# Performance work log

Measured on AMD Instinct MI355X. Metric: run time of the kernel, lower is better.

## Reference

```python
import jax, jax.numpy as jnp
import numpy as np

B, S, HLEN, VLEN, HID = 32, 2048, 1024, 1024, 1024


def setup_inputs() -> dict:
    key = jax.random.key(0)
    ks = jax.random.split(key, 6)
    scale_W = 1.0 / np.sqrt(HLEN)
    scale_U = 1.0 / np.sqrt(VLEN)
    scale_w = 1.0 / np.sqrt(HID)
    return {
        "h": jax.random.normal(ks[0], (B, HLEN), dtype=jnp.float32),
        "V": jax.random.normal(ks[1], (B, S, VLEN), dtype=jnp.float32),
        "W_w": jax.random.normal(ks[2], (HID, HLEN), dtype=jnp.float32) * scale_W,
        "W_b": jax.random.normal(ks[3], (HID,), dtype=jnp.float32) * scale_W,
        "U_w": jax.random.normal(ks[4], (HID, VLEN), dtype=jnp.float32) * scale_U,
        "w_w": jax.random.normal(ks[5], (HID,), dtype=jnp.float32) * scale_w,
    }


def reference(h, V, W_w, W_b, U_w, w_w):
    # e = w^T tanh(W h + U V^T + b); beta = softmax(e); out = sum_s beta_s V_s
    h_proj = h @ W_w.T + W_b                      # [B, HID]
    V_proj = jnp.einsum('bsv,dv->bsd', V, U_w)    # [B, S, HID]
    e = jnp.einsum('bsd,d->bs', jnp.tanh(h_proj[:, None, :] + V_proj), w_w)  # [B, S]
    beta = jax.nn.softmax(e, axis=1)              # [B, S]
    return jnp.einsum('bs,bsv->bv', beta, V)      # [B, VLEN]
```

## Files before the change

kernel.cpp:

```cpp
#include <hip/hip_runtime.h>

constexpr int B_   = 32;
constexpr int S_   = 2048;
constexpr int HID_ = 1024;
constexpr int VL_  = 1024;

typedef __attribute__((ext_vector_type(4))) float  f32x4;
typedef __attribute__((ext_vector_type(4))) short  s16x4;
typedef __attribute__((ext_vector_type(8))) short  s16x8;

__device__ __forceinline__ short f2bf(float f) {
    union { float f; unsigned u; } v; v.f = f;
    unsigned r = v.u + 0x7fffu + ((v.u >> 16) & 1u);
    return (short)(r >> 16);
}

__device__ __forceinline__ float bf2f(short s) {
    union { unsigned u; float f; } v;
    v.u = ((unsigned)(unsigned short)s) << 16;
    return v.f;
}

__device__ __forceinline__ float fast_tanh(float x) {
    float e2 = __expf(2.0f * x);
    return 1.0f - 2.0f / (e2 + 1.0f);
}

__device__ __forceinline__ void async_cp16(const void* g, void* l) {
    __builtin_amdgcn_global_load_lds(
        (const __attribute__((address_space(1))) unsigned int*)g,
        (__attribute__((address_space(3))) unsigned int*)l,
        16, 0, 0);
}

__global__ __launch_bounds__(256) void hproj_kernel(const float* __restrict__ h,
                                                    const float* __restrict__ Ww,
                                                    const float* __restrict__ Wb,
                                                    float* __restrict__ hp) {
    int tid = threadIdx.x;
    int wave = tid >> 6, lane = tid & 63;
    int d = blockIdx.x * 4 + wave;
    const float* wr = Ww + (size_t)d * HID_;
    float4 wreg[4];
#pragma unroll
    for (int i = 0; i < 4; i++) wreg[i] = *(const float4*)(wr + i * 256 + lane * 4);
    float bias = Wb[d];
    for (int b = 0; b < B_; b++) {
        const float* hr = h + (size_t)b * HID_;
        float acc = 0.0f;
#pragma unroll
        for (int i = 0; i < 4; i++) {
            float4 x = *(const float4*)(hr + i * 256 + lane * 4);
            acc += wreg[i].x * x.x + wreg[i].y * x.y + wreg[i].z * x.z + wreg[i].w * x.w;
        }
#pragma unroll
        for (int o = 32; o; o >>= 1) acc += __shfl_xor(acc, o);
        if (lane == 0) hp[(size_t)b * HID_ + d] = acc + bias;
    }
}

__global__ __launch_bounds__(256) void cvt_kernel(const float* __restrict__ src,
                                                  short* __restrict__ dst, size_t n4) {
    size_t i = (size_t)blockIdx.x * blockDim.x + threadIdx.x;
    size_t stride = (size_t)gridDim.x * blockDim.x;
    for (; i < n4; i += stride) {
        float4 x = ((const float4*)src)[i];
        s16x4 y;
        y.x = f2bf(x.x); y.y = f2bf(x.y); y.z = f2bf(x.z); y.w = f2bf(x.w);
        ((s16x4*)dst)[i] = y;
    }
}

__global__ __launch_bounds__(256) void e_kernel_bf16(const short* __restrict__ Vm,
                                                     const short* __restrict__ Um,
                                                     const float* __restrict__ hp,
                                                     const float* __restrict__ ww,
                                                     float* __restrict__ e) {
    __shared__ short As[128][32];
    __shared__ short Bs[128][32];
    __shared__ float ebuf[2][128];

    int tid = threadIdx.x;
    int s0 = blockIdx.x * 128;
    int b  = blockIdx.y;
    int wave = tid >> 6, lane = tid & 63;
    int wm = wave >> 1, wn = wave & 1;
    int col = lane & 15, quad = lane >> 4;

    int r0 = 32 * wave + (lane >> 2);
    int kc = (lane & 3) * 8;
    const short* gAb = Vm + ((size_t)b * S_ + s0 + r0) * VL_ + kc;
    short* lA0 = &As[32 * wave][0];
    short* lA1 = &As[32 * wave + 16][0];
    short* lB0 = &Bs[32 * wave][0];
    short* lB1 = &Bs[32 * wave + 16][0];

    float ep[4][4];
#pragma unroll
    for (int i = 0; i < 4; i++)
#pragma unroll
        for (int j = 0; j < 4; j++) ep[i][j] = 0.0f;

    for (int dt = 0; dt < 8; dt++) {
        int d0 = dt * 128;
        const short* gA0 = gAb;
        const short* gA1 = gAb + 16 * (size_t)VL_;
        const short* gB0 = Um + ((size_t)d0 + r0) * VL_ + kc;
        const short* gB1 = gB0 + 16 * (size_t)VL_;

        f32x4 zero = {0.f, 0.f, 0.f, 0.f};
        f32x4 acc[4][4];
#pragma unroll
        for (int i = 0; i < 4; i++)
#pragma unroll
            for (int j = 0; j < 4; j++) acc[i][j] = zero;

        for (int k0 = 0; k0 < VL_; k0 += 32) {
            async_cp16(gA0, lA0);
            async_cp16(gA1, lA1);
            async_cp16(gB0, lB0);
            async_cp16(gB1, lB1);
            gA0 += 32; gA1 += 32; gB0 += 32; gB1 += 32;
            __syncthreads();

            s16x8 a8[4], b8[4];
#pragma unroll
            for (int tm = 0; tm < 4; tm++)
                a8[tm] = *(const s16x8*)&As[wm * 64 + tm * 16 + col][quad * 8];
#pragma unroll
            for (int tn = 0; tn < 4; tn++)
                b8[tn] = *(const s16x8*)&Bs[wn * 64 + tn * 16 + col][quad * 8];
#pragma unroll
            for (int tm = 0; tm < 4; tm++)
#pragma unroll
                for (int tn = 0; tn < 4; tn++)
                    acc[tm][tn] = __builtin_amdgcn_mfma_f32_16x16x32_bf16(
                        a8[tm], b8[tn], acc[tm][tn], 0, 0, 0);
            __syncthreads();
        }

        float wv[4], hv[4];
#pragma unroll
        for (int tn = 0; tn < 4; tn++) {
            int d = d0 + wn * 64 + tn * 16 + col;
            wv[tn] = ww[d];
            hv[tn] = hp[(size_t)b * HID_ + d];
        }
#pragma unroll
        for (int tm = 0; tm < 4; tm++)
#pragma unroll
            for (int reg = 0; reg < 4; reg++) {
#pragma unroll
                for (int tn = 0; tn < 4; tn++)
                    ep[tm][reg] += wv[tn] * fast_tanh(hv[tn] + acc[tm][tn][reg]);
            }
    }

#pragma unroll
    for (int tm = 0; tm < 4; tm++)
#pragma unroll
        for (int reg = 0; reg < 4; reg++) {
            float p = ep[tm][reg];
            p += __shfl_xor(p, 1);
            p += __shfl_xor(p, 2);
            p += __shfl_xor(p, 4);
            p += __shfl_xor(p, 8);
            if (col == 0)
                ebuf[wn][wm * 64 + tm * 16 + quad * 4 + reg] = p;
        }
    __syncthreads();
    if (tid < 128)
        e[(size_t)b * S_ + s0 + tid] = ebuf[0][tid] + ebuf[1][tid];
}

__global__ __launch_bounds__(256) void e_kernel_f32(const float* __restrict__ Vm,
                                                    const float* __restrict__ Um,
                                                    const float* __restrict__ hp,
                                                    const float* __restrict__ ww,
                                                    float* __restrict__ e) {
    __shared__ short As[128][40];
    __shared__ short Bs[128][40];
    int tid = threadIdx.x;
    int b  = blockIdx.z;
    int d0 = blockIdx.x * 128;
    int s0 = blockIdx.y * 128;
    int wave = tid >> 6, lane = tid & 63;
    int wm = wave >> 1, wn = wave & 1;
    int col = lane & 15, quad = lane >> 4;

    f32x4 zero = {0.f, 0.f, 0.f, 0.f};
    f32x4 acc[4][4];
#pragma unroll
    for (int i = 0; i < 4; i++)
#pragma unroll
        for (int j = 0; j < 4; j++) acc[i][j] = zero;

    const float* Abase = Vm + ((size_t)b * S_ + s0) * (size_t)VL_;
    const float* Bbase = Um + (size_t)d0 * (size_t)VL_;

    for (int k0 = 0; k0 < VL_; k0 += 32) {
        int k4 = tid & 7, rb = tid >> 3;
#pragma unroll
        for (int i = 0; i < 4; i++) {
            int r = rb + 32 * i;
            float4 x = *(const float4*)(Abase + (size_t)r * VL_ + k0 + k4 * 4);
            s16x4 ya; ya.x = f2bf(x.x); ya.y = f2bf(x.y); ya.z = f2bf(x.z); ya.w = f2bf(x.w);
            *(s16x4*)&As[r][k4 * 4] = ya;
            float4 y = *(const float4*)(Bbase + (size_t)r * VL_ + k0 + k4 * 4);
            s16x4 yb; yb.x = f2bf(y.x); yb.y = f2bf(y.y); yb.z = f2bf(y.z); yb.w = f2bf(y.w);
            *(s16x4*)&Bs[r][k4 * 4] = yb;
        }
        __syncthreads();
        s16x8 a8[4], b8[4];
#pragma unroll
        for (int tm = 0; tm < 4; tm++)
            a8[tm] = *(const s16x8*)&As[wm * 64 + tm * 16 + col][quad * 8];
#pragma unroll
        for (int tn = 0; tn < 4; tn++)
            b8[tn] = *(const s16x8*)&Bs[wn * 64 + tn * 16 + col][quad * 8];
#pragma unroll
        for (int tm = 0; tm < 4; tm++)
#pragma unroll
            for (int tn = 0; tn < 4; tn++)
                acc[tm][tn] = __builtin_amdgcn_mfma_f32_16x16x32_bf16(
                    a8[tm], b8[tn], acc[tm][tn], 0, 0, 0);
        __syncthreads();
    }

    float wv[4], hv[4];
#pragma unroll
    for (int tn = 0; tn < 4; tn++) {
        int d = d0 + wn * 64 + tn * 16 + col;
        wv[tn] = ww[d];
        hv[tn] = hp[(size_t)b * HID_ + d];
    }
#pragma unroll
    for (int tm = 0; tm < 4; tm++) {
#pragma unroll
        for (int reg = 0; reg < 4; reg++) {
            float p = 0.0f;
#pragma unroll
            for (int tn = 0; tn < 4; tn++)
                p += wv[tn] * fast_tanh(hv[tn] + acc[tm][tn][reg]);
            p += __shfl_xor(p, 1);
            p += __shfl_xor(p, 2);
            p += __shfl_xor(p, 4);
            p += __shfl_xor(p, 8);
            if (col == 0) {
                int s = s0 + wm * 64 + tm * 16 + quad * 4 + reg;
                atomicAdd(&e[(size_t)b * S_ + s], p);
            }
        }
    }
}

__global__ __launch_bounds__(256) void softmax_kernel(float* __restrict__ e) {
    int b = blockIdx.x, tid = threadIdx.x;
    float* row = e + (size_t)b * S_;
    float v[8];
    float m = -1e30f;
#pragma unroll
    for (int i = 0; i < 8; i++) { v[i] = row[tid + i * 256]; m = fmaxf(m, v[i]); }
#pragma unroll
    for (int o = 32; o; o >>= 1) m = fmaxf(m, __shfl_xor(m, o));
    __shared__ float rm[4], rs[4];
    int wave = tid >> 6, lane = tid & 63;
    if (lane == 0) rm[wave] = m;
    __syncthreads();
    m = fmaxf(fmaxf(rm[0], rm[1]), fmaxf(rm[2], rm[3]));
    float s = 0.0f;
#pragma unroll
    for (int i = 0; i < 8; i++) { v[i] = __expf(v[i] - m); s += v[i]; }
#pragma unroll
    for (int o = 32; o; o >>= 1) s += __shfl_xor(s, o);
    if (lane == 0) rs[wave] = s;
    __syncthreads();
    s = rs[0] + rs[1] + rs[2] + rs[3];
    float inv = 1.0f / s;
#pragma unroll
    for (int i = 0; i < 8; i++) row[tid + i * 256] = v[i] * inv;
}

__global__ __launch_bounds__(256) void out_kernel_bf16(const float* __restrict__ beta,
                                                       const short* __restrict__ Vb16,
                                                       float* __restrict__ out) {
    int b = blockIdx.x, sc = blockIdx.y;
    int v4 = threadIdx.x;
    const short* Vp = Vb16 + ((size_t)b * S_ + (size_t)sc * 128) * VL_;
    const float* bb = beta + (size_t)b * S_ + (size_t)sc * 128;
    float ax = 0.f, ay = 0.f, az = 0.f, aw = 0.f;
    for (int s = 0; s < 128; s++) {
        float w = bb[s];
        s16x4 x = *(const s16x4*)(Vp + (size_t)s * VL_ + v4 * 4);
        ax += w * bf2f(x.x); ay += w * bf2f(x.y);
        az += w * bf2f(x.z); aw += w * bf2f(x.w);
    }
    float* o = out + (size_t)b * VL_ + v4 * 4;
    atomicAdd(o + 0, ax);
    atomicAdd(o + 1, ay);
    atomicAdd(o + 2, az);
    atomicAdd(o + 3, aw);
}

__global__ __launch_bounds__(256) void out_kernel_f32(const float* __restrict__ beta,
                                                      const float* __restrict__ V,
                                                      float* __restrict__ out) {
    int b = blockIdx.x, sc = blockIdx.y;
    int v4 = threadIdx.x;
    const float* Vb = V + ((size_t)b * S_ + (size_t)sc * 128) * VL_;
    const float* bb = beta + (size_t)b * S_ + (size_t)sc * 128;
    float ax = 0.f, ay = 0.f, az = 0.f, aw = 0.f;
    for (int s = 0; s < 128; s++) {
        float w = bb[s];
        float4 x = *(const float4*)(Vb + (size_t)s * VL_ + v4 * 4);
        ax += w * x.x; ay += w * x.y; az += w * x.z; aw += w * x.w;
    }
    float* o = out + (size_t)b * VL_ + v4 * 4;
    atomicAdd(o + 0, ax);
    atomicAdd(o + 1, ay);
    atomicAdd(o + 2, az);
    atomicAdd(o + 3, aw);
}

extern "C" void kernel_launch(void* const* d_in, const int* in_sizes, int n_in,
                              void* d_out, int out_size, void* d_ws, size_t ws_size,
                              hipStream_t stream) {
    const float* h  = (const float*)d_in[0];
    const float* V  = (const float*)d_in[1];
    const float* Ww = (const float*)d_in[2];
    const float* Wb = (const float*)d_in[3];
    const float* Uw = (const float*)d_in[4];
    const float* ww = (const float*)d_in[5];
    float* out = (float*)d_out;

    char* ws = (char*)d_ws;
    float* hp = (float*)ws;
    float* e  = (float*)(ws + 131072);
    short* Vb16 = (short*)(ws + 393216);
    short* Ub16 = Vb16 + (size_t)B_ * S_ * VL_;
    size_t need = 393216 + ((size_t)B_ * S_ * VL_ + (size_t)HID_ * VL_) * 2;
    bool bf16path = (ws_size >= need);

    hipMemsetAsync(out, 0, (size_t)out_size * 4, stream);

    hproj_kernel<<<dim3(HID_ / 4), 256, 0, stream>>>(h, Ww, Wb, hp);

    if (bf16path) {
        cvt_kernel<<<2048, 256, 0, stream>>>(V, Vb16, (size_t)B_ * S_ * VL_ / 4);
        cvt_kernel<<<256, 256, 0, stream>>>(Uw, Ub16, (size_t)HID_ * VL_ / 4);
        e_kernel_bf16<<<dim3(S_ / 128, B_), 256, 0, stream>>>(Vb16, Ub16, hp, ww, e);
        softmax_kernel<<<B_, 256, 0, stream>>>(e);
        out_kernel_bf16<<<dim3(B_, S_ / 128), 256, 0, stream>>>(e, Vb16, out);
    } else {
        hipMemsetAsync(e, 0, (size_t)B_ * S_ * 4, stream);
        e_kernel_f32<<<dim3(HID_ / 128, S_ / 128, B_), 256, 0, stream>>>(
            V, Uw, hp, ww, e);
        softmax_kernel<<<B_, 256, 0, stream>>>(e);
        out_kernel_f32<<<dim3(B_, S_ / 128), 256, 0, stream>>>(e, V, out);
    }
}
```

Baseline: 666.3 us.

## Split e-kernel over hidden dim halves and replace output atomics with partial reduction

The bf16 e kernel grid gains a third dimension that splits the hidden dimension into two halves. This doubles the block count from 512 to 1024 for better occupancy across CUs, and each half writes its own partial e buffer, which the softmax kernel sums. The output kernel now writes per-chunk partial sums that a new reduction kernel combines, instead of using atomics, which also removes the output memset. The V conversion launch uses more blocks. In exchange there is one extra launch and each V tile is reloaded by both hidden-dim halves.

```diff
diff --git a/kernel.cpp b/kernel.cpp
--- a/kernel.cpp
+++ b/kernel.cpp
@@ -75,14 +75,15 @@
                                                      const short* __restrict__ Um,
                                                      const float* __restrict__ hp,
                                                      const float* __restrict__ ww,
-                                                     float* __restrict__ e) {
+                                                     float* __restrict__ epart) {
     __shared__ short As[128][32];
     __shared__ short Bs[128][32];
     __shared__ float ebuf[2][128];
 
     int tid = threadIdx.x;
-    int s0 = blockIdx.x * 128;
-    int b  = blockIdx.y;
+    int dh = blockIdx.x;
+    int s0 = blockIdx.y * 128;
+    int b  = blockIdx.z;
     int wave = tid >> 6, lane = tid & 63;
     int wm = wave >> 1, wn = wave & 1;
     int col = lane & 15, quad = lane >> 4;
@@ -101,7 +102,7 @@
 #pragma unroll
         for (int j = 0; j < 4; j++) ep[i][j] = 0.0f;
 
-    for (int dt = 0; dt < 8; dt++) {
+    for (int dt = dh * 4; dt < dh * 4 + 4; dt++) {
         int d0 = dt * 128;
         const short* gA0 = gAb;
         const short* gA1 = gAb + 16 * (size_t)VL_;
@@ -170,7 +171,7 @@
         }
     __syncthreads();
     if (tid < 128)
-        e[(size_t)b * S_ + s0 + tid] = ebuf[0][tid] + ebuf[1][tid];
+        epart[((size_t)dh * B_ + b) * S_ + s0 + tid] = ebuf[0][tid] + ebuf[1][tid];
 }
 
 __global__ __launch_bounds__(256) void e_kernel_f32(const float* __restrict__ Vm,
@@ -254,13 +255,20 @@
     }
 }
 
-__global__ __launch_bounds__(256) void softmax_kernel(float* __restrict__ e) {
+__global__ __launch_bounds__(256) void softmax_kernel(const float* __restrict__ epart,
+                                                      float* __restrict__ beta,
+                                                      int nparts) {
     int b = blockIdx.x, tid = threadIdx.x;
-    float* row = e + (size_t)b * S_;
+    const float* r0 = epart + (size_t)b * S_;
+    const float* r1 = epart + ((size_t)B_ + b) * S_;
     float v[8];
     float m = -1e30f;
 #pragma unroll
-    for (int i = 0; i < 8; i++) { v[i] = row[tid + i * 256]; m = fmaxf(m, v[i]); }
+    for (int i = 0; i < 8; i++) {
+        int idx = tid + i * 256;
+        v[i] = r0[idx] + (nparts > 1 ? r1[idx] : 0.0f);
+        m = fmaxf(m, v[i]);
+    }
 #pragma unroll
     for (int o = 32; o; o >>= 1) m = fmaxf(m, __shfl_xor(m, o));
     __shared__ float rm[4], rs[4];
@@ -278,12 +286,12 @@
     s = rs[0] + rs[1] + rs[2] + rs[3];
     float inv = 1.0f / s;
 #pragma unroll
-    for (int i = 0; i < 8; i++) row[tid + i * 256] = v[i] * inv;
+    for (int i = 0; i < 8; i++) beta[(size_t)b * S_ + tid + i * 256] = v[i] * inv;
 }
 
 __global__ __launch_bounds__(256) void out_kernel_bf16(const float* __restrict__ beta,
                                                        const short* __restrict__ Vb16,
-                                                       float* __restrict__ out) {
+                                                       float* __restrict__ opart) {
     int b = blockIdx.x, sc = blockIdx.y;
     int v4 = threadIdx.x;
     const short* Vp = Vb16 + ((size_t)b * S_ + (size_t)sc * 128) * VL_;
@@ -295,11 +303,21 @@
         ax += w * bf2f(x.x); ay += w * bf2f(x.y);
         az += w * bf2f(x.z); aw += w * bf2f(x.w);
     }
-    float* o = out + (size_t)b * VL_ + v4 * 4;
-    atomicAdd(o + 0, ax);
-    atomicAdd(o + 1, ay);
-    atomicAdd(o + 2, az);
-    atomicAdd(o + 3, aw);
+    float4 r = {ax, ay, az, aw};
+    *(float4*)(opart + (((size_t)b * 16 + sc) * VL_) + v4 * 4) = r;
+}
+
+__global__ __launch_bounds__(256) void out_reduce_kernel(const float* __restrict__ opart,
+                                                         float* __restrict__ out) {
+    int b = blockIdx.x, v4 = threadIdx.x;
+    float4 a = {0.f, 0.f, 0.f, 0.f};
+    const float* base = opart + (size_t)b * 16 * VL_;
+#pragma unroll
+    for (int sc = 0; sc < 16; sc++) {
+        float4 x = *(const float4*)(base + (size_t)sc * VL_ + v4 * 4);
+        a.x += x.x; a.y += x.y; a.z += x.z; a.w += x.w;
+    }
+    *(float4*)(out + (size_t)b * VL_ + v4 * 4) = a;
 }
 
 __global__ __launch_bounds__(256) void out_kernel_f32(const float* __restrict__ beta,
@@ -334,28 +352,31 @@
     float* out = (float*)d_out;
 
     char* ws = (char*)d_ws;
-    float* hp = (float*)ws;
-    float* e  = (float*)(ws + 131072);
-    short* Vb16 = (short*)(ws + 393216);
+    float* hp    = (float*)ws;
+    float* epart = (float*)(ws + 131072);
+    float* beta  = (float*)(ws + 131072 + 524288);
+    float* opart = (float*)(ws + 131072 + 524288 + 262144);
+    size_t fixed = 131072 + 524288 + 262144 + 2097152;
+    short* Vb16 = (short*)(ws + fixed);
     short* Ub16 = Vb16 + (size_t)B_ * S_ * VL_;
-    size_t need = 393216 + ((size_t)B_ * S_ * VL_ + (size_t)HID_ * VL_) * 2;
+    size_t need = fixed + ((size_t)B_ * S_ * VL_ + (size_t)HID_ * VL_) * 2;
     bool bf16path = (ws_size >= need);
 
-    hipMemsetAsync(out, 0, (size_t)out_size * 4, stream);
-
     hproj_kernel<<<dim3(HID_ / 4), 256, 0, stream>>>(h, Ww, Wb, hp);
 
     if (bf16path) {
-        cvt_kernel<<<2048, 256, 0, stream>>>(V, Vb16, (size_t)B_ * S_ * VL_ / 4);
+        cvt_kernel<<<4096, 256, 0, stream>>>(V, Vb16, (size_t)B_ * S_ * VL_ / 4);
         cvt_kernel<<<256, 256, 0, stream>>>(Uw, Ub16, (size_t)HID_ * VL_ / 4);
-        e_kernel_bf16<<<dim3(S_ / 128, B_), 256, 0, stream>>>(Vb16, Ub16, hp, ww, e);
-        softmax_kernel<<<B_, 256, 0, stream>>>(e);
-        out_kernel_bf16<<<dim3(B_, S_ / 128), 256, 0, stream>>>(e, Vb16, out);
+        e_kernel_bf16<<<dim3(2, S_ / 128, B_), 256, 0, stream>>>(Vb16, Ub16, hp, ww, epart);
+        softmax_kernel<<<B_, 256, 0, stream>>>(epart, beta, 2);
+        out_kernel_bf16<<<dim3(B_, S_ / 128), 256, 0, stream>>>(beta, Vb16, opart);
+        out_reduce_kernel<<<B_, 256, 0, stream>>>(opart, out);
     } else {
-        hipMemsetAsync(e, 0, (size_t)B_ * S_ * 4, stream);
+        hipMemsetAsync(epart, 0, (size_t)B_ * S_ * 4, stream);
+        hipMemsetAsync(out, 0, (size_t)out_size * 4, stream);
         e_kernel_f32<<<dim3(HID_ / 128, S_ / 128, B_), 256, 0, stream>>>(
-            V, Uw, hp, ww, e);
-        softmax_kernel<<<B_, 256, 0, stream>>>(e);
-        out_kernel_f32<<<dim3(B_, S_ / 128), 256, 0, stream>>>(e, V, out);
-    }
-}
+            V, Uw, hp, ww, epart);
+        softmax_kernel<<<B_, 256, 0, stream>>>(epart, beta, 1);
+        out_kernel_f32<<<dim3(B_, S_ / 128), 256, 0, stream>>>(beta, V, out);
+    }
+}
```

After: 663.9 us. About the same (-0.4%).
